# Optimization experiments

Measured on AMD Instinct MI355X. Metric: run time of the kernel, lower is better.

Reference implementation:

```python
import jax, jax.numpy as jnp
import numpy as np

N = 100000
IN_F = 165
HID = 128
E = 1600000


def gcn_conv(x, W, b, src, dst, n):
    # PyG GCNConv: h = x @ W; add self-loops; symmetric norm D^-1/2 A D^-1/2; aggregate; + bias
    h = x @ W  # [n, out]
    src_sl = jnp.concatenate([src, jnp.arange(n)])
    dst_sl = jnp.concatenate([dst, jnp.arange(n)])
    deg = jax.ops.segment_sum(jnp.ones_like(src_sl, dtype=h.dtype), dst_sl, num_segments=n)
    dinv = jnp.where(deg > 0, jax.lax.rsqrt(deg), 0.0)
    norm = dinv[src_sl] * dinv[dst_sl]  # [e+n]
    msg = h[src_sl] * norm[:, None]
    out = jax.ops.segment_sum(msg, dst_sl, num_segments=n)
    return out + b


def setup_inputs() -> dict:
    key = jax.random.key(0)
    k = jax.random.split(key, 8)
    x = jax.random.normal(k[0], (N, IN_F), dtype=jnp.float32)
    edge_index = jax.random.randint(k[1], (2, E), 0, N)
    s1 = 1.0 / np.sqrt(IN_F)
    s2 = 1.0 / np.sqrt(HID)
    W1 = jax.random.uniform(k[2], (IN_F, HID), jnp.float32, -s1, s1)
    b1 = jnp.zeros((HID,), jnp.float32)
    W2 = jax.random.uniform(k[3], (HID, HID), jnp.float32, -s2, s2)
    b2 = jnp.zeros((HID,), jnp.float32)
    Wc = jax.random.uniform(k[4], (HID, 2), jnp.float32, -s2, s2)
    bc = jax.random.uniform(k[5], (2,), jnp.float32, -s2, s2)
    return {"x": x, "edge_index": edge_index, "W1": W1, "b1": b1,
            "W2": W2, "b2": b2, "Wc": Wc, "bc": bc}


def reference(x, edge_index, W1, b1, W2, b2, Wc, bc):
    src, dst = edge_index[0], edge_index[1]
    h = jax.nn.relu(gcn_conv(x, W1, b1, src, dst, N))
    # dropout inactive (eval mode)
    h = jax.nn.relu(gcn_conv(h, W2, b2, src, dst, N))
    return h @ Wc + bc
```

## Files before the change

kernel.cpp:

```cpp
#include <hip/hip_runtime.h>


typedef _Float16 half8 __attribute__((ext_vector_type(8)));
typedef float floatx4 __attribute__((ext_vector_type(4)));
typedef float f4u __attribute__((ext_vector_type(4), aligned(4)));

#define SLOT_C 64
#define BCAP 4608
#define NBKT 391
#define CHUNK 4096

__global__ __launch_bounds__(256) void multisplit_k(const int* __restrict__ src,
                                                    const int* __restrict__ dst, int e,
                                                    int* __restrict__ bcnt,
                                                    int2* __restrict__ edges2) {
  __shared__ int lhist[NBKT];
  __shared__ int lbase[NBKT];
  __shared__ int lcur[NBKT];
  int t = threadIdx.x;
  int e0 = blockIdx.x * CHUNK;
  int e1 = min(e0 + CHUNK, e);
  for (int b = t; b < NBKT; b += 256) { lhist[b] = 0; lcur[b] = 0; }
  __syncthreads();
  for (int i = e0 + t; i < e1; i += 256)
    atomicAdd(&lhist[dst[i] >> 8], 1);
  __syncthreads();
  for (int b = t; b < NBKT; b += 256) {
    int h = lhist[b];
    lbase[b] = h ? atomicAdd(&bcnt[b], h) : 0;
  }
  __syncthreads();
  for (int i = e0 + t; i < e1; i += 256) {
    int d = dst[i];
    int b = d >> 8;
    int p = lbase[b] + atomicAdd(&lcur[b], 1);
    if (p < BCAP) edges2[(size_t)b * BCAP + p] = make_int2(src[i], d);
  }
}

__global__ __launch_bounds__(256) void csr_from_bins_k(const int2* __restrict__ edges2,
                                                       const int* __restrict__ bcnt,
                                                       int* __restrict__ csr,
                                                       float* __restrict__ dinv, int n) {
  __shared__ int lcnt[256];
  int b = blockIdx.x;
  int node0 = b << 8;
  int t = threadIdx.x;
  lcnt[t] = 0;
  __syncthreads();
  int ec = min(bcnt[b], BCAP);
  const int2* ebase = edges2 + (size_t)b * BCAP;
  for (int i = t; i < ec; i += 256) {
    int2 ed = ebase[i];
    int p = atomicAdd(&lcnt[ed.y - node0], 1);
    if (p < SLOT_C - 1) csr[((size_t)ed.y << 6) + p] = ed.x;
  }
  __syncthreads();
  int node = node0 + t;
  if (node < n) {
    int c = lcnt[t];
    csr[((size_t)node << 6) + (SLOT_C - 1)] = c;
    dinv[node] = rsqrtf((float)(c + 1));
  }
}

__global__ void w_split_frag_k(const float* __restrict__ W, int K, int nslab,
                               _Float16* __restrict__ WF) {
  int idx = blockIdx.x * blockDim.x + threadIdx.x;
  if (idx >= nslab * 8192) return;
  int j = idx & 7;
  int lane = (idx >> 3) & 63;
  int p = (idx >> 9) & 1;
  int c = (idx >> 10) & 7;
  int s = idx >> 13;
  int k = (s << 5) + ((lane >> 4) << 3) + j;
  int col = (c << 4) + (lane & 15);
  float v = (k < K) ? W[(size_t)k * 128 + col] : 0.f;
  _Float16 h = (_Float16)v;
  WF[idx] = p ? (_Float16)(v - (float)h) : h;
}

template <bool AHALF, int NSLAB>
__global__ __launch_bounds__(256) void gemm_f16_k(const void* __restrict__ Av,
                                                  const _Float16* __restrict__ WF,
                                                  const float* __restrict__ rowscale,
                                                  _Float16* __restrict__ out,
                                                  int n, int K) {
  int wave = threadIdx.x >> 6, lane = threadIdx.x & 63;
  int m = lane & 15, quad = lane >> 4;
  int rowbase = blockIdx.x * 128 + wave * 32;
  int ra[2];
  ra[0] = min(rowbase + m, n - 1);
  ra[1] = min(rowbase + 16 + m, n - 1);

  floatx4 acc[2][8];
#pragma unroll
  for (int t = 0; t < 2; ++t)
#pragma unroll
    for (int c = 0; c < 8; ++c) acc[t][c] = (floatx4){0.f, 0.f, 0.f, 0.f};

  f4u xb[3][2][2];
  half8 hb[3][2];

  auto loadA = [&](int s, int b) {
    int k0 = (s << 5) + quad * 8;
#pragma unroll
    for (int t = 0; t < 2; ++t) {
      if constexpr (AHALF) {
        const _Float16* arow = (const _Float16*)Av + (size_t)ra[t] * K;
        hb[b][t] = *(const half8*)(arow + k0);
      } else {
        const float* arow = (const float*)Av + (size_t)ra[t] * K;
        if ((s << 5) + 32 <= K) {
          xb[b][t][0] = *(const f4u*)(arow + k0);
          xb[b][t][1] = *(const f4u*)(arow + k0 + 4);
        } else {
#pragma unroll
          for (int j = 0; j < 4; ++j) { int kk = k0 + j;     kk = kk < K ? kk : K - 1; xb[b][t][0][j] = arow[kk]; }
#pragma unroll
          for (int j = 0; j < 4; ++j) { int kk = k0 + 4 + j; kk = kk < K ? kk : K - 1; xb[b][t][1][j] = arow[kk]; }
        }
      }
    }
  };

  loadA(0, 0);
  if (NSLAB > 1) loadA(1, 1);

#pragma unroll
  for (int s = 0; s < NSLAB; ++s) {
    const _Float16* wbase = WF + (size_t)s * 8192;
    half8 wh[8], wl[8];
#pragma unroll
    for (int c = 0; c < 8; ++c) {
      wh[c] = *(const half8*)(wbase + c * 1024 + lane * 8);
      wl[c] = *(const half8*)(wbase + c * 1024 + 512 + lane * 8);
    }
    if (s + 2 < NSLAB) loadA(s + 2, (s + 2) % 3);

    int b = s % 3;
    half8 ah[2], al[2];
#pragma unroll
    for (int t = 0; t < 2; ++t) {
      if constexpr (AHALF) {
        ah[t] = hb[b][t];
      } else {
#pragma unroll
        for (int j = 0; j < 8; ++j) {
          float v = (j < 4) ? xb[b][t][0][j] : xb[b][t][1][j - 4];
          _Float16 hh = (_Float16)v;
          ah[t][j] = hh;
          al[t][j] = (_Float16)(v - (float)hh);
        }
      }
    }
#pragma unroll
    for (int c = 0; c < 8; ++c)
#pragma unroll
      for (int t = 0; t < 2; ++t) {
        acc[t][c] = __builtin_amdgcn_mfma_f32_16x16x32_f16(ah[t], wh[c], acc[t][c], 0, 0, 0);
        acc[t][c] = __builtin_amdgcn_mfma_f32_16x16x32_f16(ah[t], wl[c], acc[t][c], 0, 0, 0);
        if constexpr (!AHALF)
          acc[t][c] = __builtin_amdgcn_mfma_f32_16x16x32_f16(al[t], wh[c], acc[t][c], 0, 0, 0);
      }
  }

#pragma unroll
  for (int t = 0; t < 2; ++t) {
#pragma unroll
    for (int i = 0; i < 4; ++i) {
      int row = rowbase + t * 16 + quad * 4 + i;
      if (row < n) {
        float di = rowscale ? rowscale[row] : 1.0f;
#pragma unroll
        for (int c = 0; c < 8; ++c)
          out[(size_t)row * 128 + c * 16 + m] = (_Float16)(acc[t][c][i] * di);
      }
    }
  }
}

template <bool CLS>
__global__ __launch_bounds__(256) void aggregate_k(const _Float16* __restrict__ g,
                                                   const int* __restrict__ csr,
                                                   const float* __restrict__ dinv,
                                                   const float* __restrict__ bias,
                                                   const float* __restrict__ Wc,
                                                   const float* __restrict__ bc,
                                                   _Float16* __restrict__ out16,
                                                   float* __restrict__ out32, int n) {
  int wave = threadIdx.x >> 6;
  int lane = threadIdx.x & 63;
  int i = blockIdx.x * 4 + wave;
  if (i >= n) return;
  int qtr = lane >> 4;
  int l16 = lane & 15;
  int f = l16 * 8;

  int sv = csr[((size_t)i << 6) + lane];
  half8 self = *(const half8*)&g[(size_t)i * 128 + f];
  float di = dinv[i];
  float4 b0 = *(const float4*)&bias[f];
  float4 b1 = *(const float4*)&bias[f + 4];

  int deg = min(__shfl(sv, SLOT_C - 1, 64), SLOT_C - 1);

  float acc[8];
#pragma unroll
  for (int j = 0; j < 8; ++j) acc[j] = 0.f;

  auto grp = [&](int k) {
    int ee = 4 * k + qtr;
    bool valid = ee < deg;
    int ec = valid ? ee : 0;
    int srow = __shfl(sv, ec, 64);
    half8 v = *(const half8*)&g[(size_t)srow * 128 + f];
    float w = valid ? 1.f : 0.f;
#pragma unroll
    for (int j = 0; j < 8; ++j) acc[j] = fmaf(w, (float)v[j], acc[j]);
  };

  if (deg > 0) {
    if (deg <= 16) {
#pragma unroll
      for (int k = 0; k < 4; ++k) grp(k);
    } else if (deg <= 32) {
#pragma unroll
      for (int k = 0; k < 8; ++k) grp(k);
    } else {
#pragma unroll
      for (int k = 0; k < 16; ++k) grp(k);
    }
#pragma unroll
    for (int j = 0; j < 8; ++j) {
      acc[j] += __shfl_xor(acc[j], 16, 64);
      acc[j] += __shfl_xor(acc[j], 32, 64);
    }
  }

  float bv[8] = {b0.x, b0.y, b0.z, b0.w, b1.x, b1.y, b1.z, b1.w};
  float r[8];
#pragma unroll
  for (int j = 0; j < 8; ++j)
    r[j] = fmaxf((acc[j] + (float)self[j]) * di + bv[j], 0.f);

  if (!CLS) {
    if (qtr == 0) {
      half8 o;
#pragma unroll
      for (int j = 0; j < 8; ++j) o[j] = (_Float16)(r[j] * di);
      *(half8*)&out16[(size_t)i * 128 + f] = o;
    }
  } else {
    float c0v = 0.f, c1v = 0.f;
#pragma unroll
    for (int q = 0; q < 4; ++q) {
      float4 wv = *(const float4*)&Wc[f * 2 + q * 4];
      c0v += r[q * 2] * wv.x + r[q * 2 + 1] * wv.z;
      c1v += r[q * 2] * wv.y + r[q * 2 + 1] * wv.w;
    }
#pragma unroll
    for (int off = 8; off > 0; off >>= 1) {
      c0v += __shfl_down(c0v, off, 16);
      c1v += __shfl_down(c1v, off, 16);
    }
    if (lane == 0) {
      out32[(size_t)i * 2 + 0] = c0v + bc[0];
      out32[(size_t)i * 2 + 1] = c1v + bc[1];
    }
  }
}

extern "C" void kernel_launch(void* const* d_in, const int* in_sizes, int n_in,
                              void* d_out, int out_size, void* d_ws, size_t ws_size,
                              hipStream_t stream) {
  const float* x  = (const float*)d_in[0];
  const int*   ei = (const int*)d_in[1];
  const float* W1 = (const float*)d_in[2];
  const float* b1 = (const float*)d_in[3];
  const float* W2 = (const float*)d_in[4];
  const float* b2 = (const float*)d_in[5];
  const float* Wc = (const float*)d_in[6];
  const float* bc = (const float*)d_in[7];
  float* out = (float*)d_out;

  const int IN_F = 165;
  const int NS1 = 6;
  const int NS2 = 4;
  const int n = in_sizes[0] / IN_F;
  const int e = in_sizes[1] / 2;
  const int* src = ei;
  const int* dst = ei + e;

  char* ws = (char*)d_ws;
  size_t off = 0;
  auto alloc = [&](size_t bytes) -> void* {
    void* p = ws + off;
    off += (bytes + 255) & ~(size_t)255;
    return p;
  };
  _Float16* bufA = (_Float16*)alloc((size_t)n * 128 * 2);
  _Float16* bufB = (_Float16*)alloc((size_t)n * 128 * 2);
  int*   csr  = (int*)alloc((size_t)n * SLOT_C * 4);
  int2*  edges2 = (int2*)alloc((size_t)NBKT * BCAP * 8);
  int*   bcnt = (int*)alloc((size_t)NBKT * 4);
  float* dinv = (float*)alloc((size_t)n * 4);
  _Float16* wf1 = (_Float16*)alloc((size_t)NS1 * 8192 * 2);
  _Float16* wf2 = (_Float16*)alloc((size_t)NS2 * 8192 * 2);

  hipMemsetAsync(bcnt, 0, (size_t)NBKT * 4, stream);

  w_split_frag_k<<<NS1 * 32, 256, 0, stream>>>(W1, IN_F, NS1, wf1);
  w_split_frag_k<<<NS2 * 32, 256, 0, stream>>>(W2, 128, NS2, wf2);

  multisplit_k<<<(e + CHUNK - 1) / CHUNK, 256, 0, stream>>>(src, dst, e, bcnt, edges2);
  csr_from_bins_k<<<NBKT, 256, 0, stream>>>(edges2, bcnt, csr, dinv, n);

  const int gemmgrid = (n + 127) / 128;
  gemm_f16_k<false, NS1><<<gemmgrid, 256, 0, stream>>>(x, wf1, dinv, bufA, n, IN_F);
  aggregate_k<false><<<(n + 3) / 4, 256, 0, stream>>>(bufA, csr, dinv, b1, nullptr, nullptr,
                                                      bufB, nullptr, n);
  gemm_f16_k<true, NS2><<<gemmgrid, 256, 0, stream>>>(bufB, wf2, nullptr, bufA, n, 128);
  aggregate_k<true><<<(n + 3) / 4, 256, 0, stream>>>(bufA, csr, dinv, b2, Wc, bc,
                                                     nullptr, out, n);
}
```

Measured before the change: 342.2 us.

## Fuse layer-1 GEMM with edge binning and W2 prep in one launch

```diff
diff --git a/kernel.cpp b/kernel.cpp
--- a/kernel.cpp
+++ b/kernel.cpp
@@ -2,6 +2,7 @@
 
 
 typedef _Float16 half8 __attribute__((ext_vector_type(8)));
+typedef _Float16 half4 __attribute__((ext_vector_type(4)));
 typedef float floatx4 __attribute__((ext_vector_type(4)));
 typedef float f4u __attribute__((ext_vector_type(4), aligned(4)));
 
@@ -10,57 +11,161 @@
 #define NBKT 391
 #define CHUNK 4096
 
-__global__ __launch_bounds__(256) void multisplit_k(const int* __restrict__ src,
-                                                    const int* __restrict__ dst, int e,
-                                                    int* __restrict__ bcnt,
-                                                    int2* __restrict__ edges2) {
+template <bool AHALF, int NSLAB, bool OUT32>
+__device__ __forceinline__ void gemm_body(int bid, const void* __restrict__ Av,
+                                          const _Float16* __restrict__ WF,
+                                          const float* __restrict__ rowscale,
+                                          void* __restrict__ outv, int n, int K) {
+  int wave = threadIdx.x >> 6, lane = threadIdx.x & 63;
+  int m = lane & 15, quad = lane >> 4;
+  int rowbase = bid * 128 + wave * 32;
+  int ra[2];
+  ra[0] = min(rowbase + m, n - 1);
+  ra[1] = min(rowbase + 16 + m, n - 1);
+
+  floatx4 acc[2][8];
+#pragma unroll
+  for (int t = 0; t < 2; ++t)
+#pragma unroll
+    for (int c = 0; c < 8; ++c) acc[t][c] = (floatx4){0.f, 0.f, 0.f, 0.f};
+
+  f4u xb[3][2][2];
+  half8 hb[3][2];
+
+  auto loadA = [&](int s, int b) {
+    int k0 = (s << 5) + quad * 8;
+#pragma unroll
+    for (int t = 0; t < 2; ++t) {
+      if constexpr (AHALF) {
+        const _Float16* arow = (const _Float16*)Av + (size_t)ra[t] * K;
+        hb[b][t] = *(const half8*)(arow + k0);
+      } else {
+        const float* arow = (const float*)Av + (size_t)ra[t] * K;
+        if ((s << 5) + 32 <= K) {
+          xb[b][t][0] = *(const f4u*)(arow + k0);
+          xb[b][t][1] = *(const f4u*)(arow + k0 + 4);
+        } else {
+#pragma unroll
+          for (int j = 0; j < 4; ++j) { int kk = k0 + j;     kk = kk < K ? kk : K - 1; xb[b][t][0][j] = arow[kk]; }
+#pragma unroll
+          for (int j = 0; j < 4; ++j) { int kk = k0 + 4 + j; kk = kk < K ? kk : K - 1; xb[b][t][1][j] = arow[kk]; }
+        }
+      }
+    }
+  };
+
+  loadA(0, 0);
+  if (NSLAB > 1) loadA(1, 1);
+
+#pragma unroll
+  for (int s = 0; s < NSLAB; ++s) {
+    const _Float16* wbase = WF + (size_t)s * 8192;
+    half8 wh[8], wl[8];
+#pragma unroll
+    for (int c = 0; c < 8; ++c) {
+      wh[c] = *(const half8*)(wbase + c * 1024 + lane * 8);
+      wl[c] = *(const half8*)(wbase + c * 1024 + 512 + lane * 8);
+    }
+    if (s + 2 < NSLAB) loadA(s + 2, (s + 2) % 3);
+
+    int b = s % 3;
+    half8 ah[2], al[2];
+#pragma unroll
+    for (int t = 0; t < 2; ++t) {
+      if constexpr (AHALF) {
+        ah[t] = hb[b][t];
+      } else {
+#pragma unroll
+        for (int j = 0; j < 8; ++j) {
+          float v = (j < 4) ? xb[b][t][0][j] : xb[b][t][1][j - 4];
+          _Float16 hh = (_Float16)v;
+          ah[t][j] = hh;
+          al[t][j] = (_Float16)(v - (float)hh);
+        }
+      }
+    }
+#pragma unroll
+    for (int c = 0; c < 8; ++c)
+#pragma unroll
+      for (int t = 0; t < 2; ++t) {
+        acc[t][c] = __builtin_amdgcn_mfma_f32_16x16x32_f16(ah[t], wh[c], acc[t][c], 0, 0, 0);
+        acc[t][c] = __builtin_amdgcn_mfma_f32_16x16x32_f16(ah[t], wl[c], acc[t][c], 0, 0, 0);
+        if constexpr (!AHALF)
+          acc[t][c] = __builtin_amdgcn_mfma_f32_16x16x32_f16(al[t], wh[c], acc[t][c], 0, 0, 0);
+      }
+  }
+
+#pragma unroll
+  for (int t = 0; t < 2; ++t) {
+#pragma unroll
+    for (int i = 0; i < 4; ++i) {
+      int row = rowbase + t * 16 + quad * 4 + i;
+      if (row < n) {
+        float di = rowscale ? rowscale[row] : 1.0f;
+#pragma unroll
+        for (int c = 0; c < 8; ++c) {
+          if constexpr (OUT32)
+            ((float*)outv)[(size_t)row * 128 + c * 16 + m] = acc[t][c][i] * di;
+          else
+            ((_Float16*)outv)[(size_t)row * 128 + c * 16 + m] = (_Float16)(acc[t][c][i] * di);
+        }
+      }
+    }
+  }
+}
+
+__global__ __launch_bounds__(256) void front_k(const float* __restrict__ x,
+                                               const _Float16* __restrict__ wf1,
+                                               float* __restrict__ g1raw, int n, int K,
+                                               const int* __restrict__ src,
+                                               const int* __restrict__ dst, int e,
+                                               int* __restrict__ bcnt,
+                                               int2* __restrict__ edges2,
+                                               const float* __restrict__ W2,
+                                               _Float16* __restrict__ wf2,
+                                               int gg, int ms) {
   __shared__ int lhist[NBKT];
   __shared__ int lbase[NBKT];
   __shared__ int lcur[NBKT];
   int t = threadIdx.x;
-  int e0 = blockIdx.x * CHUNK;
-  int e1 = min(e0 + CHUNK, e);
-  for (int b = t; b < NBKT; b += 256) { lhist[b] = 0; lcur[b] = 0; }
-  __syncthreads();
-  for (int i = e0 + t; i < e1; i += 256)
-    atomicAdd(&lhist[dst[i] >> 8], 1);
-  __syncthreads();
-  for (int b = t; b < NBKT; b += 256) {
-    int h = lhist[b];
-    lbase[b] = h ? atomicAdd(&bcnt[b], h) : 0;
-  }
-  __syncthreads();
-  for (int i = e0 + t; i < e1; i += 256) {
-    int d = dst[i];
-    int b = d >> 8;
-    int p = lbase[b] + atomicAdd(&lcur[b], 1);
-    if (p < BCAP) edges2[(size_t)b * BCAP + p] = make_int2(src[i], d);
-  }
-}
-
-__global__ __launch_bounds__(256) void csr_from_bins_k(const int2* __restrict__ edges2,
-                                                       const int* __restrict__ bcnt,
-                                                       int* __restrict__ csr,
-                                                       float* __restrict__ dinv, int n) {
-  __shared__ int lcnt[256];
-  int b = blockIdx.x;
-  int node0 = b << 8;
-  int t = threadIdx.x;
-  lcnt[t] = 0;
-  __syncthreads();
-  int ec = min(bcnt[b], BCAP);
-  const int2* ebase = edges2 + (size_t)b * BCAP;
-  for (int i = t; i < ec; i += 256) {
-    int2 ed = ebase[i];
-    int p = atomicAdd(&lcnt[ed.y - node0], 1);
-    if (p < SLOT_C - 1) csr[((size_t)ed.y << 6) + p] = ed.x;
-  }
-  __syncthreads();
-  int node = node0 + t;
-  if (node < n) {
-    int c = lcnt[t];
-    csr[((size_t)node << 6) + (SLOT_C - 1)] = c;
-    dinv[node] = rsqrtf((float)(c + 1));
+  int blk = blockIdx.x;
+
+  if (blk < gg) {
+    gemm_body<false, 6, true>(blk, x, wf1, nullptr, g1raw, n, K);
+  } else if (blk < gg + ms) {
+    int mb = blk - gg;
+    int e0 = mb * CHUNK;
+    int e1 = min(e0 + CHUNK, e);
+    for (int b = t; b < NBKT; b += 256) { lhist[b] = 0; lcur[b] = 0; }
+    __syncthreads();
+    for (int i = e0 + t; i < e1; i += 256)
+      atomicAdd(&lhist[dst[i] >> 8], 1);
+    __syncthreads();
+    for (int b = t; b < NBKT; b += 256) {
+      int h = lhist[b];
+      lbase[b] = h ? atomicAdd(&bcnt[b], h) : 0;
+    }
+    __syncthreads();
+    for (int i = e0 + t; i < e1; i += 256) {
+      int d = dst[i];
+      int b = d >> 8;
+      int p = lbase[b] + atomicAdd(&lcur[b], 1);
+      if (p < BCAP) edges2[(size_t)b * BCAP + p] = make_int2(src[i], d);
+    }
+  } else {
+    int idx = (blk - gg - ms) * 256 + t;
+    if (idx < 4 * 8192) {
+      int j = idx & 7;
+      int lane = (idx >> 3) & 63;
+      int p = (idx >> 9) & 1;
+      int c = (idx >> 10) & 7;
+      int s = idx >> 13;
+      int k = (s << 5) + ((lane >> 4) << 3) + j;
+      int col = (c << 4) + (lane & 15);
+      float v = W2[(size_t)k * 128 + col];
+      _Float16 h = (_Float16)v;
+      wf2[idx] = p ? (_Float16)(v - (float)h) : h;
+    }
   }
 }
 
@@ -80,104 +185,57 @@
   WF[idx] = p ? (_Float16)(v - (float)h) : h;
 }
 
-template <bool AHALF, int NSLAB>
-__global__ __launch_bounds__(256) void gemm_f16_k(const void* __restrict__ Av,
-                                                  const _Float16* __restrict__ WF,
-                                                  const float* __restrict__ rowscale,
-                                                  _Float16* __restrict__ out,
-                                                  int n, int K) {
-  int wave = threadIdx.x >> 6, lane = threadIdx.x & 63;
-  int m = lane & 15, quad = lane >> 4;
-  int rowbase = blockIdx.x * 128 + wave * 32;
-  int ra[2];
-  ra[0] = min(rowbase + m, n - 1);
-  ra[1] = min(rowbase + 16 + m, n - 1);
-
-  floatx4 acc[2][8];
-#pragma unroll
-  for (int t = 0; t < 2; ++t)
-#pragma unroll
-    for (int c = 0; c < 8; ++c) acc[t][c] = (floatx4){0.f, 0.f, 0.f, 0.f};
-
-  f4u xb[3][2][2];
-  half8 hb[3][2];
-
-  auto loadA = [&](int s, int b) {
-    int k0 = (s << 5) + quad * 8;
-#pragma unroll
-    for (int t = 0; t < 2; ++t) {
-      if constexpr (AHALF) {
-        const _Float16* arow = (const _Float16*)Av + (size_t)ra[t] * K;
-        hb[b][t] = *(const half8*)(arow + k0);
-      } else {
-        const float* arow = (const float*)Av + (size_t)ra[t] * K;
-        if ((s << 5) + 32 <= K) {
-          xb[b][t][0] = *(const f4u*)(arow + k0);
-          xb[b][t][1] = *(const f4u*)(arow + k0 + 4);
-        } else {
-#pragma unroll
-          for (int j = 0; j < 4; ++j) { int kk = k0 + j;     kk = kk < K ? kk : K - 1; xb[b][t][0][j] = arow[kk]; }
-#pragma unroll
-          for (int j = 0; j < 4; ++j) { int kk = k0 + 4 + j; kk = kk < K ? kk : K - 1; xb[b][t][1][j] = arow[kk]; }
-        }
-      }
-    }
-  };
-
-  loadA(0, 0);
-  if (NSLAB > 1) loadA(1, 1);
-
-#pragma unroll
-  for (int s = 0; s < NSLAB; ++s) {
-    const _Float16* wbase = WF + (size_t)s * 8192;
-    half8 wh[8], wl[8];
-#pragma unroll
-    for (int c = 0; c < 8; ++c) {
-      wh[c] = *(const half8*)(wbase + c * 1024 + lane * 8);
-      wl[c] = *(const half8*)(wbase + c * 1024 + 512 + lane * 8);
-    }
-    if (s + 2 < NSLAB) loadA(s + 2, (s + 2) % 3);
-
-    int b = s % 3;
-    half8 ah[2], al[2];
-#pragma unroll
-    for (int t = 0; t < 2; ++t) {
-      if constexpr (AHALF) {
-        ah[t] = hb[b][t];
-      } else {
-#pragma unroll
-        for (int j = 0; j < 8; ++j) {
-          float v = (j < 4) ? xb[b][t][0][j] : xb[b][t][1][j - 4];
-          _Float16 hh = (_Float16)v;
-          ah[t][j] = hh;
-          al[t][j] = (_Float16)(v - (float)hh);
-        }
-      }
-    }
-#pragma unroll
-    for (int c = 0; c < 8; ++c)
-#pragma unroll
-      for (int t = 0; t < 2; ++t) {
-        acc[t][c] = __builtin_amdgcn_mfma_f32_16x16x32_f16(ah[t], wh[c], acc[t][c], 0, 0, 0);
-        acc[t][c] = __builtin_amdgcn_mfma_f32_16x16x32_f16(ah[t], wl[c], acc[t][c], 0, 0, 0);
-        if constexpr (!AHALF)
-          acc[t][c] = __builtin_amdgcn_mfma_f32_16x16x32_f16(al[t], wh[c], acc[t][c], 0, 0, 0);
-      }
-  }
-
-#pragma unroll
-  for (int t = 0; t < 2; ++t) {
-#pragma unroll
-    for (int i = 0; i < 4; ++i) {
-      int row = rowbase + t * 16 + quad * 4 + i;
-      if (row < n) {
-        float di = rowscale ? rowscale[row] : 1.0f;
-#pragma unroll
-        for (int c = 0; c < 8; ++c)
-          out[(size_t)row * 128 + c * 16 + m] = (_Float16)(acc[t][c][i] * di);
-      }
-    }
-  }
+__global__ __launch_bounds__(256) void csr_bins_scale_k(const int2* __restrict__ edges2,
+                                                        const int* __restrict__ bcnt,
+                                                        int* __restrict__ csr,
+                                                        float* __restrict__ dinv,
+                                                        const float* __restrict__ g1raw,
+                                                        _Float16* __restrict__ g1, int n) {
+  __shared__ int lcnt[256];
+  __shared__ float ldinv[256];
+  int b = blockIdx.x;
+  int node0 = b << 8;
+  int t = threadIdx.x;
+  lcnt[t] = 0;
+  __syncthreads();
+  int ec = min(bcnt[b], BCAP);
+  const int2* ebase = edges2 + (size_t)b * BCAP;
+  for (int i = t; i < ec; i += 256) {
+    int2 ed = ebase[i];
+    int p = atomicAdd(&lcnt[ed.y - node0], 1);
+    if (p < SLOT_C - 1) csr[((size_t)ed.y << 6) + p] = ed.x;
+  }
+  __syncthreads();
+  int node = node0 + t;
+  float di = 0.f;
+  if (node < n) {
+    int c = lcnt[t];
+    di = rsqrtf((float)(c + 1));
+    csr[((size_t)node << 6) + (SLOT_C - 1)] = c;
+    dinv[node] = di;
+  }
+  ldinv[t] = di;
+  __syncthreads();
+  int nrows = min(256, n - node0);
+  if (nrows > 0) {
+    const f4u* rb = (const f4u*)(g1raw + (size_t)node0 * 128);
+    _Float16* wb = g1 + (size_t)node0 * 128;
+    int tot = nrows * 32;
+    for (int idx = t; idx < tot; idx += 256) {
+      float d = ldinv[idx >> 5];
+      f4u v = rb[idx];
+      half4 o;
+#pragma unroll
+      for (int j = 0; j < 4; ++j) o[j] = (_Float16)(v[j] * d);
+      *(half4*)&wb[idx * 4] = o;
+    }
+  }
+}
+
+__global__ __launch_bounds__(256) void gemm2_k(const _Float16* __restrict__ A,
+                                               const _Float16* __restrict__ WF,
+                                               _Float16* __restrict__ out, int n) {
+  gemm_body<true, 4, false>(blockIdx.x, A, WF, nullptr, out, n, 128);
 }
 
 template <bool CLS>
@@ -299,7 +357,8 @@
     off += (bytes + 255) & ~(size_t)255;
     return p;
   };
-  _Float16* bufA = (_Float16*)alloc((size_t)n * 128 * 2);
+  float*    g1raw = (float*)alloc((size_t)n * 128 * 4);
+  _Float16* g1   = (_Float16*)alloc((size_t)n * 128 * 2);
   _Float16* bufB = (_Float16*)alloc((size_t)n * 128 * 2);
   int*   csr  = (int*)alloc((size_t)n * SLOT_C * 4);
   int2*  edges2 = (int2*)alloc((size_t)NBKT * BCAP * 8);
@@ -307,20 +366,23 @@
   float* dinv = (float*)alloc((size_t)n * 4);
   _Float16* wf1 = (_Float16*)alloc((size_t)NS1 * 8192 * 2);
   _Float16* wf2 = (_Float16*)alloc((size_t)NS2 * 8192 * 2);
+  _Float16* g2 = (_Float16*)g1raw;
 
   hipMemsetAsync(bcnt, 0, (size_t)NBKT * 4, stream);
 
   w_split_frag_k<<<NS1 * 32, 256, 0, stream>>>(W1, IN_F, NS1, wf1);
-  w_split_frag_k<<<NS2 * 32, 256, 0, stream>>>(W2, 128, NS2, wf2);
-
-  multisplit_k<<<(e + CHUNK - 1) / CHUNK, 256, 0, stream>>>(src, dst, e, bcnt, edges2);
-  csr_from_bins_k<<<NBKT, 256, 0, stream>>>(edges2, bcnt, csr, dinv, n);
-
-  const int gemmgrid = (n + 127) / 128;
-  gemm_f16_k<false, NS1><<<gemmgrid, 256, 0, stream>>>(x, wf1, dinv, bufA, n, IN_F);
-  aggregate_k<false><<<(n + 3) / 4, 256, 0, stream>>>(bufA, csr, dinv, b1, nullptr, nullptr,
+
+  const int GG = (n + 127) / 128;
+  const int MS = (e + CHUNK - 1) / CHUNK;
+  const int WS2 = NS2 * 32;
+  front_k<<<GG + MS + WS2, 256, 0, stream>>>(x, wf1, g1raw, n, IN_F,
+                                             src, dst, e, bcnt, edges2,
+                                             W2, wf2, GG, MS);
+  csr_bins_scale_k<<<NBKT, 256, 0, stream>>>(edges2, bcnt, csr, dinv, g1raw, g1, n);
+
+  aggregate_k<false><<<(n + 3) / 4, 256, 0, stream>>>(g1, csr, dinv, b1, nullptr, nullptr,
                                                       bufB, nullptr, n);
-  gemm_f16_k<true, NS2><<<gemmgrid, 256, 0, stream>>>(bufB, wf2, nullptr, bufA, n, 128);
-  aggregate_k<true><<<(n + 3) / 4, 256, 0, stream>>>(bufA, csr, dinv, b2, Wc, bc,
+  gemm2_k<<<GG, 256, 0, stream>>>(bufB, wf2, g2, n);
+  aggregate_k<true><<<(n + 3) / 4, 256, 0, stream>>>(g2, csr, dinv, b2, Wc, bc,
                                                      nullptr, out, n);
 }
```

Measured after the change: 354.6 us. +3.6%, slower.
